# Kernel optimization log

Measured on AMD Instinct MI355X. Metric: run time of the kernel, lower is better.

Reference implementation:

```python
import jax, jax.numpy as jnp
import numpy as np

LOG_2PI = float(np.log(2.0 * np.pi))
MASK_SCORE = -1.0e15


def setup_inputs() -> dict:
    key = jax.random.key(0)
    k1, k2, k3, k4 = jax.random.split(key, 4)
    B, H, D, T = 32, 600, 512, 2400
    encoder_outputs = jax.random.normal(k1, (B, H, D), dtype=jnp.float32)
    # per-phoneme durations in frames (float, as the torch code casts via cumsum().float())
    durations = jax.random.randint(k2, (B, H), 0, 8).astype(jnp.float32)
    # per-phoneme Gaussian variances; keep strictly positive for log(vars)
    vars_ = jax.random.uniform(k3, (B, H), dtype=jnp.float32) * 0.9 + 0.1
    input_lengths = jax.random.randint(k4, (B,), 1, H, dtype=jnp.int32)
    return {
        "encoder_outputs": encoder_outputs,
        "durations": durations,
        "vars": vars_,
        "input_lengths": input_lengths,
        "frame_length": T,
    }


def reference(encoder_outputs, durations, vars, input_lengths, frame_length):
    # encoder_outputs: [B, H, D]; durations, vars: [B, H]; input_lengths: [B]
    B, H, D = encoder_outputs.shape
    # Gaussian centers: cumulative duration minus half the phoneme's own duration
    c = jnp.cumsum(durations, axis=1) - 0.5 * durations            # [B, H]
    t = jnp.arange(frame_length, dtype=jnp.float32)                 # [T]
    # log N(t; c, vars): [B, H, T]
    diff = t[None, None, :] - c[:, :, None]
    w_t = -0.5 * (LOG_2PI + jnp.log(vars)[:, :, None] + diff * diff / vars[:, :, None])
    # mask out padded phoneme positions (h >= input_length)
    pad_mask = jnp.arange(H)[None, :] >= input_lengths[:, None]     # [B, H]
    w_t = jnp.where(pad_mask[:, :, None], MASK_SCORE, w_t)
    # softmax over the phoneme (hidden) axis
    w_t = jax.nn.softmax(w_t, axis=1)                                # [B, H, T]
    # upsample: [B, T, H] @ [B, H, D] -> [B, T, D]
    return jnp.einsum("bht,bhd->btd", w_t, encoder_outputs)
```

## Files before the change

### kernel.cpp

```cpp
#include <hip/hip_runtime.h>
#include <hip/hip_bf16.h>

using f32x4   = __attribute__((ext_vector_type(4))) float;
using short8  = __attribute__((ext_vector_type(8))) short;
using short4v = __attribute__((ext_vector_type(4))) short;

#define LOG2_2PI 2.6514961294723187f
#define L2E_HALF 0.7213475204444817f
#define HP2 640

__device__ __forceinline__ short bf16bits(float x) {
  unsigned u = __builtin_bit_cast(unsigned, x);
  u = (u + 0x7FFFu + ((u >> 16) & 1u)) >> 16;
  return (short)u;
}
__device__ __forceinline__ float bf16round(float x) {
  unsigned u = __builtin_bit_cast(unsigned, x);
  u = ((u + 0x7FFFu + ((u >> 16) & 1u)) >> 16) << 16;
  return __builtin_bit_cast(float, u);
}

__global__ void prep_kernel(const float* __restrict__ dur,
                            const float* __restrict__ vars,
                            const int* __restrict__ lens,
                            f32x4* __restrict__ pk, float* __restrict__ aux,
                            int H) {
  const int b = blockIdx.x;
  const int l = threadIdx.x;
  const int L = lens[b];
  float run = 0.f, prevD = 0.f;
  float Gmax = 0.f, qMin = 1e30f, qMax = 0.f, bMin = 1e30f, bMax = -1e30f;
  for (int h0 = 0; h0 < HP2; h0 += 64) {
    const int h = h0 + l;
    const float d = (h < H) ? dur[(size_t)b * H + h] : 0.f;
    float x = d;
#pragma unroll
    for (int off = 1; off < 64; off <<= 1) {
      float y = __shfl_up(x, off);
      if (l >= off) x += y;
    }
    float dp = __shfl_up(d, 1);
    if (l == 0) dp = prevD;
    f32x4 e = (f32x4){0.f, 0.f, -1e30f, 0.f};
    if (h < H) {
      const float v = vars[(size_t)b * H + h];
      const float q = L2E_HALF / v;
      const float bc = -0.5f * (LOG2_2PI + __builtin_amdgcn_logf(v));
      e[0] = run + x - 0.5f * d;
      e[1] = q;
      e[2] = (h < L) ? bc : -1e30f;
      if (h < L) {
        qMin = fminf(qMin, q); qMax = fmaxf(qMax, q);
        bMin = fminf(bMin, bc); bMax = fmaxf(bMax, bc);
        if (h >= 1) Gmax = fmaxf(Gmax, 0.5f * (d + dp));
      }
    }
    pk[(size_t)b * HP2 + h] = e;
    prevD = __shfl(d, 63);
    run += __shfl(x, 63);
  }
#pragma unroll
  for (int off = 1; off < 64; off <<= 1) {
    qMin = fminf(qMin, __shfl_xor(qMin, off));
    qMax = fmaxf(qMax, __shfl_xor(qMax, off));
    bMin = fminf(bMin, __shfl_xor(bMin, off));
    bMax = fmaxf(bMax, __shfl_xor(bMax, off));
    Gmax = fmaxf(Gmax, __shfl_xor(Gmax, off));
  }
  if (l == 0) {
    float* ax = aux + b * 8;
    ax[0] = Gmax; ax[1] = qMin; ax[2] = qMax; ax[3] = bMin; ax[4] = bMax;
  }
}

__global__ void win_kernel(const f32x4* __restrict__ pk,
                           const float* __restrict__ aux,
                           const int* __restrict__ lens,
                           int* __restrict__ win, int T, int TT) {
  const int b = blockIdx.x;
  const int L = lens[b];
  const float Gmax = aux[b * 8 + 0], qMn = aux[b * 8 + 1], qMx = aux[b * 8 + 2];
  const float bMn  = aux[b * 8 + 3], bMx = aux[b * 8 + 4];
  const f32x4* pc = pk + (size_t)b * HP2;
  const float c0 = pc[0][0], cL = pc[L - 1][0];
  for (int tile = threadIdx.x; tile < TT; tile += blockDim.x) {
    const float tLo = (float)(tile * 32);
    const float tHi = (float)(min(tile * 32 + 31, T - 1));
    const float D0 = fmaxf(0.5f * Gmax, fmaxf(fmaxf(c0 - tLo, tHi - cL), 0.f));
    const float Wr = __fsqrt_rn(((bMx - bMn) + 65.f + qMx * D0 * D0) / qMn);
    int lo = 0, hi = L;
    const float thLo = tLo - Wr;
    while (lo < hi) { const int mid = (lo + hi) >> 1; if (pc[mid][0] < thLo) lo = mid + 1; else hi = mid; }
    int hLo = lo;
    int lo2 = hLo, hi2 = L;
    const float thHi = tHi + Wr;
    while (lo2 < hi2) { const int mid = (lo2 + hi2) >> 1; if (pc[mid][0] <= thHi) lo2 = mid + 1; else hi2 = mid; }
    int hHi = lo2;
    if (hHi <= hLo) { hLo = max(hLo - 1, 0); hHi = min(hLo + 2, L); }
    win[(b * TT + tile) * 2 + 0] = hLo >> 6;
    win[(b * TT + tile) * 2 + 1] = (hHi + 63) >> 6;
  }
}

__global__ void transpose_kernel(const float* __restrict__ enc,
                                 short* __restrict__ encT,
                                 int H, int D) {
  __shared__ short sT[64][66];
  const int b  = blockIdx.z;
  const int h0 = blockIdx.y * 64;
  const int d0 = blockIdx.x * 64;
  const int tid = threadIdx.x;

  const int dc = (tid & 15) * 4;
  const int hr = tid >> 4;
#pragma unroll
  for (int ps = 0; ps < 4; ++ps) {
    const int hh = hr + ps * 16;
    const int h  = h0 + hh;
    f32x4 v = (h < H) ? *(const f32x4*)&enc[((size_t)b * H + h) * D + d0 + dc]
                      : (f32x4){0.f, 0.f, 0.f, 0.f};
#pragma unroll
    for (int j = 0; j < 4; ++j) sT[dc + j][hh] = bf16bits(v[j]);
  }
  __syncthreads();

  const int tx4 = (tid & 15) * 4;
  const int ty2 = tid >> 4;
#pragma unroll
  for (int i = 0; i < 4; ++i) {
    const int d = d0 + ty2 + i * 16;
    short4v v;
#pragma unroll
    for (int j = 0; j < 4; ++j) v[j] = sT[ty2 + i * 16][tx4 + j];
    *(short4v*)&encT[((size_t)b * D + d) * HP2 + h0 + tx4] = v;
  }
}

__launch_bounds__(256, 3)
__global__ void gup_kernel(const short* __restrict__ encT,
                           const f32x4* __restrict__ pk,
                           const int* __restrict__ win,
                           float* __restrict__ out,
                           int T, int TT) {
  constexpr int D  = 512;
  constexpr int AS = 72;

  __shared__ __align__(16) float sc[HP2], sq[HP2], sb[HP2];
  __shared__ float sden[32];
  __shared__ short sA[2][32 * AS];

  const int tid   = threadIdx.x;
  const int b     = blockIdx.y;
  const int tIdx  = blockIdx.x >> 1;
  const int t0    = tIdx * 32;
  const int dbase = (blockIdx.x & 1) * 256;

  const int cLo = win[(b * TT + tIdx) * 2 + 0];
  const int cHi = win[(b * TT + tIdx) * 2 + 1];
  const int base = cLo * 64;
  const int nC   = cHi - cLo;
  const int W64  = nC * 64;

  for (int i = tid; i < W64; i += 256) {
    const f32x4 v = pk[(size_t)b * HP2 + base + i];
    sc[i] = v[0]; sq[i] = v[1]; sb[i] = v[2];
  }
  __syncthreads();

  const int tfA = tid >> 3;
  const int hs8 = tid & 7;
  const float tA = (float)(t0 + tfA);
  float mA = -1e30f;
  for (int h4 = hs8 * 4; h4 < W64; h4 += 32) {
    const f32x4 cv = *(const f32x4*)&sc[h4];
    const f32x4 qv = *(const f32x4*)&sq[h4];
    const f32x4 bv = *(const f32x4*)&sb[h4];
#pragma unroll
    for (int j = 0; j < 4; ++j) {
      const float dd = tA - cv[j];
      mA = fmaxf(mA, fmaf(-dd * dd, qv[j], bv[j]));
    }
  }
  mA = fmaxf(mA, __shfl_xor(mA, 1));
  mA = fmaxf(mA, __shfl_xor(mA, 2));
  mA = fmaxf(mA, __shfl_xor(mA, 4));

  const int lane = tid & 63;
  const int wv   = tid >> 6;
  const int l15  = lane & 15;
  const int lq   = lane >> 4;

  f32x4 acc[2][4];
#pragma unroll
  for (int i = 0; i < 2; ++i)
#pragma unroll
    for (int j = 0; j < 4; ++j) acc[i][j] = (f32x4){0.f, 0.f, 0.f, 0.f};

  const int k8 = hs8 * 8;
  float denAcc = 0.f;
  const short* bp = encT + ((size_t)b * D + dbase + wv * 64 + l15) * HP2 + base + lq * 8;

  int p = 0;
  for (int cc = 0; cc < nC; ++cc) {
    const int hb = cc * 64 + k8;
    const f32x4 cv0 = *(const f32x4*)&sc[hb];
    const f32x4 qv0 = *(const f32x4*)&sq[hb];
    const f32x4 bv0 = *(const f32x4*)&sb[hb];
    const f32x4 cv1 = *(const f32x4*)&sc[hb + 4];
    const f32x4 qv1 = *(const f32x4*)&sq[hb + 4];
    const f32x4 bv1 = *(const f32x4*)&sb[hb + 4];
    short8 w;
    float denAdd = 0.f, pmax = 0.f;
#pragma unroll
    for (int j = 0; j < 4; ++j) {
      const float dd = tA - cv0[j];
      const float pv = __builtin_amdgcn_exp2f(fmaf(-dd * dd, qv0[j], bv0[j]) - mA);
      w[j] = bf16bits(pv);
      denAdd += bf16round(pv);
      pmax = fmaxf(pmax, pv);
    }
#pragma unroll
    for (int j = 0; j < 4; ++j) {
      const float dd = tA - cv1[j];
      const float pv = __builtin_amdgcn_exp2f(fmaf(-dd * dd, qv1[j], bv1[j]) - mA);
      w[4 + j] = bf16bits(pv);
      denAdd += bf16round(pv);
      pmax = fmaxf(pmax, pv);
    }

    if (!__syncthreads_or(pmax > 1e-20f)) continue;

    denAcc += denAdd;
    *(short8*)&sA[p][tfA * AS + k8] = w;
    __syncthreads();

#pragma unroll
    for (int kh = 0; kh < 2; ++kh) {
      short8 bfv[4];
#pragma unroll
      for (int nt = 0; nt < 4; ++nt)
        bfv[nt] = *(const short8*)(bp + (size_t)nt * 16 * HP2 + cc * 64 + kh * 32);
      short8 af[2];
#pragma unroll
      for (int mt = 0; mt < 2; ++mt)
        af[mt] = *(short8*)&sA[p][(mt * 16 + l15) * AS + kh * 32 + lq * 8];
#pragma unroll
      for (int mt = 0; mt < 2; ++mt)
#pragma unroll
        for (int nt = 0; nt < 4; ++nt)
          acc[mt][nt] = __builtin_amdgcn_mfma_f32_16x16x32_bf16(bfv[nt], af[mt], acc[mt][nt], 0, 0, 0);
    }
    p ^= 1;
  }

  {
    float dsum = denAcc;
    dsum += __shfl_xor(dsum, 1);
    dsum += __shfl_xor(dsum, 2);
    dsum += __shfl_xor(dsum, 4);
    if (hs8 == 0) sden[tfA] = dsum;
  }
  __syncthreads();

#pragma unroll
  for (int mt = 0; mt < 2; ++mt) {
    const int tg = t0 + mt * 16 + l15;
    const float inv = 1.0f / sden[mt * 16 + l15];
    if (tg < T) {
#pragma unroll
      for (int nt = 0; nt < 4; ++nt) {
        f32x4 o;
#pragma unroll
        for (int i = 0; i < 4; ++i) o[i] = acc[mt][nt][i] * inv;
        *(f32x4*)&out[((size_t)b * T + tg) * D + dbase + wv * 64 + nt * 16 + lq * 4] = o;
      }
    }
  }
}

extern "C" void kernel_launch(void* const* d_in, const int* in_sizes, int n_in,
                              void* d_out, int out_size, void* d_ws, size_t ws_size,
                              hipStream_t stream) {
  const float* enc  = (const float*)d_in[0];
  const float* dur  = (const float*)d_in[1];
  const float* vars = (const float*)d_in[2];
  const int*   lens = (const int*)d_in[3];

  const int B = in_sizes[3];
  const int H = in_sizes[1] / B;
  const int D = in_sizes[0] / in_sizes[1];
  const int T = out_size / (B * D);
  const int TT = (T + 31) / 32;
  (void)n_in; (void)ws_size;

  f32x4* pk  = (f32x4*)d_ws;
  float* aux = (float*)(pk + (size_t)B * HP2);
  int*   wn  = (int*)(aux + 8 * (size_t)B);
  short* encT = (short*)(wn + (size_t)B * TT * 2);

  prep_kernel<<<B, 64, 0, stream>>>(dur, vars, lens, pk, aux, H);

  win_kernel<<<B, 128, 0, stream>>>(pk, aux, lens, wn, T, TT);

  dim3 tgrid(D / 64, HP2 / 64, B);
  transpose_kernel<<<tgrid, 256, 0, stream>>>(enc, encT, H, D);

  dim3 grid(TT * 2, B);
  gup_kernel<<<grid, 256, 0, stream>>>(encT, pk, wn, (float*)d_out, T, TT);
}
```

Measured before the change: 77.74 us.

## Compute exact per-frame max and tight windows in a separate kernel

Replaces the bound-based window kernel with a per-tile kernel that scans all phonemes per frame, finds the exact row max, and sets the window to the phonemes scoring within a fixed margin of that max. The GEMM kernel then reads the precomputed max, no longer stages the parameters in LDS, and drops the per-chunk skip vote. This aims for narrower windows and less setup per GEMM block, and raises the occupancy hint from 3 to 4 blocks. The trade-off is a full O(L) scan per frame in the new kernel, done twice, plus an extra workspace array.

New measurement: 120.3 us. 54.7% more time.

```diff
diff --git a/kernel.cpp b/kernel.cpp
--- a/kernel.cpp
+++ b/kernel.cpp
@@ -23,13 +23,11 @@
 __global__ void prep_kernel(const float* __restrict__ dur,
                             const float* __restrict__ vars,
                             const int* __restrict__ lens,
-                            f32x4* __restrict__ pk, float* __restrict__ aux,
-                            int H) {
+                            f32x4* __restrict__ pk, int H) {
   const int b = blockIdx.x;
   const int l = threadIdx.x;
   const int L = lens[b];
-  float run = 0.f, prevD = 0.f;
-  float Gmax = 0.f, qMin = 1e30f, qMax = 0.f, bMin = 1e30f, bMax = -1e30f;
+  float run = 0.f;
   for (int h0 = 0; h0 < HP2; h0 += 64) {
     const int h = h0 + l;
     const float d = (h < H) ? dur[(size_t)b * H + h] : 0.f;
@@ -39,64 +37,70 @@
       float y = __shfl_up(x, off);
       if (l >= off) x += y;
     }
-    float dp = __shfl_up(d, 1);
-    if (l == 0) dp = prevD;
     f32x4 e = (f32x4){0.f, 0.f, -1e30f, 0.f};
     if (h < H) {
       const float v = vars[(size_t)b * H + h];
-      const float q = L2E_HALF / v;
-      const float bc = -0.5f * (LOG2_2PI + __builtin_amdgcn_logf(v));
       e[0] = run + x - 0.5f * d;
-      e[1] = q;
-      e[2] = (h < L) ? bc : -1e30f;
-      if (h < L) {
-        qMin = fminf(qMin, q); qMax = fmaxf(qMax, q);
-        bMin = fminf(bMin, bc); bMax = fmaxf(bMax, bc);
-        if (h >= 1) Gmax = fmaxf(Gmax, 0.5f * (d + dp));
-      }
+      e[1] = L2E_HALF / v;
+      e[2] = (h < L) ? -0.5f * (LOG2_2PI + __builtin_amdgcn_logf(v)) : -1e30f;
     }
     pk[(size_t)b * HP2 + h] = e;
-    prevD = __shfl(d, 63);
     run += __shfl(x, 63);
   }
-#pragma unroll
-  for (int off = 1; off < 64; off <<= 1) {
-    qMin = fminf(qMin, __shfl_xor(qMin, off));
-    qMax = fmaxf(qMax, __shfl_xor(qMax, off));
-    bMin = fminf(bMin, __shfl_xor(bMin, off));
-    bMax = fmaxf(bMax, __shfl_xor(bMax, off));
-    Gmax = fmaxf(Gmax, __shfl_xor(Gmax, off));
-  }
-  if (l == 0) {
-    float* ax = aux + b * 8;
-    ax[0] = Gmax; ax[1] = qMin; ax[2] = qMax; ax[3] = bMin; ax[4] = bMax;
-  }
-}
-
-__global__ void win_kernel(const f32x4* __restrict__ pk,
-                           const float* __restrict__ aux,
-                           const int* __restrict__ lens,
-                           int* __restrict__ win, int T, int TT) {
-  const int b = blockIdx.x;
-  const int L = lens[b];
-  const float Gmax = aux[b * 8 + 0], qMn = aux[b * 8 + 1], qMx = aux[b * 8 + 2];
-  const float bMn  = aux[b * 8 + 3], bMx = aux[b * 8 + 4];
+}
+
+__global__ void win2_kernel(const f32x4* __restrict__ pk,
+                            const int* __restrict__ lens,
+                            float* __restrict__ mArr, int* __restrict__ win,
+                            int T, int TT) {
+  __shared__ int sLo, sHi;
+  const int tile = blockIdx.x;
+  const int b    = blockIdx.y;
+  const int L    = lens[b];
+  const int tid  = threadIdx.x;
+  const int f    = tid >> 3;
+  const int hs   = tid & 7;
+  const int t    = tile * 32 + f;
+  const float tA = (float)t;
   const f32x4* pc = pk + (size_t)b * HP2;
-  const float c0 = pc[0][0], cL = pc[L - 1][0];
-  for (int tile = threadIdx.x; tile < TT; tile += blockDim.x) {
-    const float tLo = (float)(tile * 32);
-    const float tHi = (float)(min(tile * 32 + 31, T - 1));
-    const float D0 = fmaxf(0.5f * Gmax, fmaxf(fmaxf(c0 - tLo, tHi - cL), 0.f));
-    const float Wr = __fsqrt_rn(((bMx - bMn) + 65.f + qMx * D0 * D0) / qMn);
-    int lo = 0, hi = L;
-    const float thLo = tLo - Wr;
-    while (lo < hi) { const int mid = (lo + hi) >> 1; if (pc[mid][0] < thLo) lo = mid + 1; else hi = mid; }
-    int hLo = lo;
-    int lo2 = hLo, hi2 = L;
-    const float thHi = tHi + Wr;
-    while (lo2 < hi2) { const int mid = (lo2 + hi2) >> 1; if (pc[mid][0] <= thHi) lo2 = mid + 1; else hi2 = mid; }
-    int hHi = lo2;
-    if (hHi <= hLo) { hLo = max(hLo - 1, 0); hHi = min(hLo + 2, L); }
+
+  if (tid == 0) { sLo = L; sHi = 0; }
+
+  float m = -3.0e38f;
+  for (int h = hs; h < L; h += 8) {
+    const f32x4 v = pc[h];
+    const float dd = tA - v[0];
+    m = fmaxf(m, fmaf(-dd * dd, v[1], v[2]));
+  }
+  m = fmaxf(m, __shfl_xor(m, 1));
+  m = fmaxf(m, __shfl_xor(m, 2));
+  m = fmaxf(m, __shfl_xor(m, 4));
+
+  const float thr = m - 66.f;
+  int lo = L, hi = -1;
+  for (int h = hs; h < L; h += 8) {
+    const f32x4 v = pc[h];
+    const float dd = tA - v[0];
+    const float s = fmaf(-dd * dd, v[1], v[2]);
+    if (s > thr) { lo = min(lo, h); hi = max(hi, h); }
+  }
+  lo = min(lo, __shfl_xor(lo, 1));
+  lo = min(lo, __shfl_xor(lo, 2));
+  lo = min(lo, __shfl_xor(lo, 4));
+  hi = max(hi, __shfl_xor(hi, 1));
+  hi = max(hi, __shfl_xor(hi, 2));
+  hi = max(hi, __shfl_xor(hi, 4));
+
+  __syncthreads();
+  if (hs == 0 && t < T) {
+    mArr[(size_t)b * TT * 32 + t] = m;
+    atomicMin(&sLo, lo);
+    atomicMax(&sHi, hi);
+  }
+  __syncthreads();
+  if (tid == 0) {
+    int hLo = sLo, hHi = sHi + 1;
+    if (hHi <= hLo) { hLo = 0; hHi = 1; }
     win[(b * TT + tile) * 2 + 0] = hLo >> 6;
     win[(b * TT + tile) * 2 + 1] = (hHi + 63) >> 6;
   }
@@ -136,16 +140,16 @@
   }
 }
 
-__launch_bounds__(256, 3)
+__launch_bounds__(256, 4)
 __global__ void gup_kernel(const short* __restrict__ encT,
                            const f32x4* __restrict__ pk,
                            const int* __restrict__ win,
+                           const float* __restrict__ mArr,
                            float* __restrict__ out,
                            int T, int TT) {
   constexpr int D  = 512;
   constexpr int AS = 72;
 
-  __shared__ __align__(16) float sc[HP2], sq[HP2], sb[HP2];
   __shared__ float sden[32];
   __shared__ short sA[2][32 * AS];
 
@@ -155,35 +159,15 @@
   const int t0    = tIdx * 32;
   const int dbase = (blockIdx.x & 1) * 256;
 
-  const int cLo = win[(b * TT + tIdx) * 2 + 0];
-  const int cHi = win[(b * TT + tIdx) * 2 + 1];
+  const int cLo  = win[(b * TT + tIdx) * 2 + 0];
+  const int nC   = win[(b * TT + tIdx) * 2 + 1] - cLo;
   const int base = cLo * 64;
-  const int nC   = cHi - cLo;
-  const int W64  = nC * 64;
-
-  for (int i = tid; i < W64; i += 256) {
-    const f32x4 v = pk[(size_t)b * HP2 + base + i];
-    sc[i] = v[0]; sq[i] = v[1]; sb[i] = v[2];
-  }
-  __syncthreads();
 
   const int tfA = tid >> 3;
   const int hs8 = tid & 7;
+  const int k8  = hs8 * 8;
   const float tA = (float)(t0 + tfA);
-  float mA = -1e30f;
-  for (int h4 = hs8 * 4; h4 < W64; h4 += 32) {
-    const f32x4 cv = *(const f32x4*)&sc[h4];
-    const f32x4 qv = *(const f32x4*)&sq[h4];
-    const f32x4 bv = *(const f32x4*)&sb[h4];
-#pragma unroll
-    for (int j = 0; j < 4; ++j) {
-      const float dd = tA - cv[j];
-      mA = fmaxf(mA, fmaf(-dd * dd, qv[j], bv[j]));
-    }
-  }
-  mA = fmaxf(mA, __shfl_xor(mA, 1));
-  mA = fmaxf(mA, __shfl_xor(mA, 2));
-  mA = fmaxf(mA, __shfl_xor(mA, 4));
+  const float mA = mArr[(size_t)b * TT * 32 + t0 + tfA];
 
   const int lane = tid & 63;
   const int wv   = tid >> 6;
@@ -196,41 +180,21 @@
 #pragma unroll
     for (int j = 0; j < 4; ++j) acc[i][j] = (f32x4){0.f, 0.f, 0.f, 0.f};
 
-  const int k8 = hs8 * 8;
   float denAcc = 0.f;
+  const f32x4* pc = pk + (size_t)b * HP2 + base + k8;
   const short* bp = encT + ((size_t)b * D + dbase + wv * 64 + l15) * HP2 + base + lq * 8;
 
   int p = 0;
-  for (int cc = 0; cc < nC; ++cc) {
-    const int hb = cc * 64 + k8;
-    const f32x4 cv0 = *(const f32x4*)&sc[hb];
-    const f32x4 qv0 = *(const f32x4*)&sq[hb];
-    const f32x4 bv0 = *(const f32x4*)&sb[hb];
-    const f32x4 cv1 = *(const f32x4*)&sc[hb + 4];
-    const f32x4 qv1 = *(const f32x4*)&sq[hb + 4];
-    const f32x4 bv1 = *(const f32x4*)&sb[hb + 4];
+  for (int cc = 0; cc < nC; ++cc, p ^= 1) {
     short8 w;
-    float denAdd = 0.f, pmax = 0.f;
-#pragma unroll
-    for (int j = 0; j < 4; ++j) {
-      const float dd = tA - cv0[j];
-      const float pv = __builtin_amdgcn_exp2f(fmaf(-dd * dd, qv0[j], bv0[j]) - mA);
+#pragma unroll
+    for (int j = 0; j < 8; ++j) {
+      const f32x4 v = pc[cc * 64 + j];
+      const float dd = tA - v[0];
+      const float pv = __builtin_amdgcn_exp2f(fmaf(-dd * dd, v[1], v[2]) - mA);
       w[j] = bf16bits(pv);
-      denAdd += bf16round(pv);
-      pmax = fmaxf(pmax, pv);
-    }
-#pragma unroll
-    for (int j = 0; j < 4; ++j) {
-      const float dd = tA - cv1[j];
-      const float pv = __builtin_amdgcn_exp2f(fmaf(-dd * dd, qv1[j], bv1[j]) - mA);
-      w[4 + j] = bf16bits(pv);
-      denAdd += bf16round(pv);
-      pmax = fmaxf(pmax, pv);
-    }
-
-    if (!__syncthreads_or(pmax > 1e-20f)) continue;
-
-    denAcc += denAdd;
+      denAcc += bf16round(pv);
+    }
     *(short8*)&sA[p][tfA * AS + k8] = w;
     __syncthreads();
 
@@ -250,7 +214,6 @@
         for (int nt = 0; nt < 4; ++nt)
           acc[mt][nt] = __builtin_amdgcn_mfma_f32_16x16x32_bf16(bfv[nt], af[mt], acc[mt][nt], 0, 0, 0);
     }
-    p ^= 1;
   }
 
   {
@@ -293,18 +256,19 @@
   const int TT = (T + 31) / 32;
   (void)n_in; (void)ws_size;
 
-  f32x4* pk  = (f32x4*)d_ws;
-  float* aux = (float*)(pk + (size_t)B * HP2);
-  int*   wn  = (int*)(aux + 8 * (size_t)B);
-  short* encT = (short*)(wn + (size_t)B * TT * 2);
-
-  prep_kernel<<<B, 64, 0, stream>>>(dur, vars, lens, pk, aux, H);
-
-  win_kernel<<<B, 128, 0, stream>>>(pk, aux, lens, wn, T, TT);
+  f32x4* pk   = (f32x4*)d_ws;
+  int*   wn   = (int*)(pk + (size_t)B * HP2);
+  float* mArr = (float*)(wn + (size_t)B * TT * 2);
+  short* encT = (short*)(mArr + (size_t)B * TT * 32);
+
+  prep_kernel<<<B, 64, 0, stream>>>(dur, vars, lens, pk, H);
+
+  dim3 wgrid(TT, B);
+  win2_kernel<<<wgrid, 256, 0, stream>>>(pk, lens, mArr, wn, T, TT);
 
   dim3 tgrid(D / 64, HP2 / 64, B);
   transpose_kernel<<<tgrid, 256, 0, stream>>>(enc, encT, H, D);
 
   dim3 grid(TT * 2, B);
-  gup_kernel<<<grid, 256, 0, stream>>>(encT, pk, wn, (float*)d_out, T, TT);
-}
+  gup_kernel<<<grid, 256, 0, stream>>>(encT, pk, wn, mArr, (float*)d_out, T, TT);
+}
```

## Fuse window search into upsample kernel and skip transposing padded phoneme tiles

Applied to the files above, without the earlier changes.

Removes the separate window kernel: each upsample block now loads the full per-batch Gaussian parameter array into shared memory, derives the valid length by searching for the masked bias values, and binary-searches its own phoneme chunk window. The transpose kernel now exits early for 64-row tiles entirely beyond the padded input length, skipping reads and writes of unused encoder rows. This saves one launch and a large part of the transpose traffic. In exchange, every block loads more shared data and repeats the searches. The old fallback for an empty window was dropped, which could matter in edge cases.

Result: slower. 80.25 us (+3.2%).

```diff
diff --git a/kernel.cpp b/kernel.cpp
--- a/kernel.cpp
+++ b/kernel.cpp
@@ -73,42 +73,16 @@
   }
 }
 
-__global__ void win_kernel(const f32x4* __restrict__ pk,
-                           const float* __restrict__ aux,
-                           const int* __restrict__ lens,
-                           int* __restrict__ win, int T, int TT) {
-  const int b = blockIdx.x;
-  const int L = lens[b];
-  const float Gmax = aux[b * 8 + 0], qMn = aux[b * 8 + 1], qMx = aux[b * 8 + 2];
-  const float bMn  = aux[b * 8 + 3], bMx = aux[b * 8 + 4];
-  const f32x4* pc = pk + (size_t)b * HP2;
-  const float c0 = pc[0][0], cL = pc[L - 1][0];
-  for (int tile = threadIdx.x; tile < TT; tile += blockDim.x) {
-    const float tLo = (float)(tile * 32);
-    const float tHi = (float)(min(tile * 32 + 31, T - 1));
-    const float D0 = fmaxf(0.5f * Gmax, fmaxf(fmaxf(c0 - tLo, tHi - cL), 0.f));
-    const float Wr = __fsqrt_rn(((bMx - bMn) + 65.f + qMx * D0 * D0) / qMn);
-    int lo = 0, hi = L;
-    const float thLo = tLo - Wr;
-    while (lo < hi) { const int mid = (lo + hi) >> 1; if (pc[mid][0] < thLo) lo = mid + 1; else hi = mid; }
-    int hLo = lo;
-    int lo2 = hLo, hi2 = L;
-    const float thHi = tHi + Wr;
-    while (lo2 < hi2) { const int mid = (lo2 + hi2) >> 1; if (pc[mid][0] <= thHi) lo2 = mid + 1; else hi2 = mid; }
-    int hHi = lo2;
-    if (hHi <= hLo) { hLo = max(hLo - 1, 0); hHi = min(hLo + 2, L); }
-    win[(b * TT + tile) * 2 + 0] = hLo >> 6;
-    win[(b * TT + tile) * 2 + 1] = (hHi + 63) >> 6;
-  }
-}
-
 __global__ void transpose_kernel(const float* __restrict__ enc,
                                  short* __restrict__ encT,
+                                 const int* __restrict__ lens,
                                  int H, int D) {
   __shared__ short sT[64][66];
   const int b  = blockIdx.z;
   const int h0 = blockIdx.y * 64;
   const int d0 = blockIdx.x * 64;
+  const int Lpad = (lens[b] + 63) & ~63;
+  if (h0 >= Lpad) return;
   const int tid = threadIdx.x;
 
   const int dc = (tid & 15) * 4;
@@ -139,7 +113,7 @@
 __launch_bounds__(256, 3)
 __global__ void gup_kernel(const short* __restrict__ encT,
                            const f32x4* __restrict__ pk,
-                           const int* __restrict__ win,
+                           const float* __restrict__ aux,
                            float* __restrict__ out,
                            int T, int TT) {
   constexpr int D  = 512;
@@ -155,23 +129,40 @@
   const int t0    = tIdx * 32;
   const int dbase = (blockIdx.x & 1) * 256;
 
-  const int cLo = win[(b * TT + tIdx) * 2 + 0];
-  const int cHi = win[(b * TT + tIdx) * 2 + 1];
-  const int base = cLo * 64;
-  const int nC   = cHi - cLo;
-  const int W64  = nC * 64;
-
-  for (int i = tid; i < W64; i += 256) {
-    const f32x4 v = pk[(size_t)b * HP2 + base + i];
+  for (int i = tid; i < HP2; i += 256) {
+    const f32x4 v = pk[(size_t)b * HP2 + i];
     sc[i] = v[0]; sq[i] = v[1]; sb[i] = v[2];
   }
   __syncthreads();
+
+  const float Gmax = aux[b * 8 + 0], qMn = aux[b * 8 + 1], qMx = aux[b * 8 + 2];
+  const float bMn  = aux[b * 8 + 3], bMx = aux[b * 8 + 4];
+  int llo = 0, lhi = HP2;
+  while (llo < lhi) { const int mid = (llo + lhi) >> 1; if (sb[mid] > -1e29f) llo = mid + 1; else lhi = mid; }
+  const int L = max(llo, 1);
+
+  const float tLo = (float)t0;
+  const float tHi = (float)(min(t0 + 31, T - 1));
+  const float c0 = sc[0], cL = sc[L - 1];
+  const float D0 = fmaxf(0.5f * Gmax, fmaxf(fmaxf(c0 - tLo, tHi - cL), 0.f));
+  const float Wr = __fsqrt_rn(((bMx - bMn) + 65.f + qMx * D0 * D0) / qMn);
+
+  int lo = 0, hi = L;
+  const float thLo = tLo - Wr;
+  while (lo < hi) { const int mid = (lo + hi) >> 1; if (sc[mid] < thLo) lo = mid + 1; else hi = mid; }
+  const int hLo = lo;
+  int lo2 = hLo, hi2 = L;
+  const float thHi = tHi + Wr;
+  while (lo2 < hi2) { const int mid = (lo2 + hi2) >> 1; if (sc[mid] <= thHi) lo2 = mid + 1; else hi2 = mid; }
+  const int hHi = lo2;
+  const int cLo = hLo >> 6;
+  const int cHi = (hHi + 63) >> 6;
 
   const int tfA = tid >> 3;
   const int hs8 = tid & 7;
   const float tA = (float)(t0 + tfA);
   float mA = -1e30f;
-  for (int h4 = hs8 * 4; h4 < W64; h4 += 32) {
+  for (int h4 = cLo * 64 + hs8 * 4; h4 < cHi * 64; h4 += 32) {
     const f32x4 cv = *(const f32x4*)&sc[h4];
     const f32x4 qv = *(const f32x4*)&sq[h4];
     const f32x4 bv = *(const f32x4*)&sb[h4];
@@ -198,10 +189,10 @@
 
   const int k8 = hs8 * 8;
   float denAcc = 0.f;
-  const short* bp = encT + ((size_t)b * D + dbase + wv * 64 + l15) * HP2 + base + lq * 8;
+  const short* bp = encT + ((size_t)b * D + dbase + wv * 64 + l15) * HP2 + lq * 8;
 
   int p = 0;
-  for (int cc = 0; cc < nC; ++cc) {
+  for (int cc = cLo; cc < cHi; ++cc) {
     const int hb = cc * 64 + k8;
     const f32x4 cv0 = *(const f32x4*)&sc[hb];
     const f32x4 qv0 = *(const f32x4*)&sq[hb];
@@ -295,16 +286,13 @@
 
   f32x4* pk  = (f32x4*)d_ws;
   float* aux = (float*)(pk + (size_t)B * HP2);
-  int*   wn  = (int*)(aux + 8 * (size_t)B);
-  short* encT = (short*)(wn + (size_t)B * TT * 2);
+  short* encT = (short*)(aux + 8 * (size_t)B);
 
   prep_kernel<<<B, 64, 0, stream>>>(dur, vars, lens, pk, aux, H);
 
-  win_kernel<<<B, 128, 0, stream>>>(pk, aux, lens, wn, T, TT);
-
   dim3 tgrid(D / 64, HP2 / 64, B);
-  transpose_kernel<<<tgrid, 256, 0, stream>>>(enc, encT, H, D);
+  transpose_kernel<<<tgrid, 256, 0, stream>>>(enc, encT, lens, H, D);
 
   dim3 grid(TT * 2, B);
-  gup_kernel<<<grid, 256, 0, stream>>>(encT, pk, wn, (float*)d_out, T, TT);
-}
+  gup_kernel<<<grid, 256, 0, stream>>>(encT, pk, aux, (float*)d_out, T, TT);
+}
```
